# Kernel tuning notes

Hardware: AMD Instinct MI355X
Metric: run time of the kernel (lower is better)

The kernel has to match this reference:

```python
import jax, jax.numpy as jnp
import numpy as np

BLOCK = 192
SCALE = 2048 ** (-0.5)


def setup_inputs() -> dict:
    key = jax.random.key(0)
    k1, k2, k3, k4 = jax.random.split(key, 4)
    B, N, C = 8, 1920, 512
    x = jax.random.normal(k1, (B, N, C), dtype=jnp.float32)
    g = jax.random.normal(k2, (B, N, C), dtype=jnp.float32)
    # nn.Linear(dim, dim, bias=False) weights, stored as [out, in] like torch
    Wq = jax.random.normal(k3, (C, C), dtype=jnp.float32) * (1.0 / np.sqrt(C))
    Wg = jax.random.normal(k4, (C, C), dtype=jnp.float32) * (1.0 / np.sqrt(C))
    return {"x": x, "g": g, "Wq": Wq, "Wg": Wg}


def reference(x, g, Wq, Wg):
    B, N, C = g.shape
    # q = x + mean over tokens of g
    q = x + jnp.mean(g, axis=1, keepdims=True)
    rel_q = jnp.einsum('bnc,dc->bnd', q, Wq)  # Linear: y = x @ W^T
    # ---- block-local cosine attention over chunks of 192 tokens ----
    gb = g.reshape(B * N // BLOCK, BLOCK, C)
    norm = jnp.linalg.norm(gb, axis=-1, keepdims=True)
    rel = gb / jnp.maximum(norm, 1e-12)  # F.normalize(dim=-1)
    scores = jnp.einsum('bic,bjc->bij', rel, rel) * SCALE  # [nb,192,192]
    attn = jax.nn.softmax(scores, axis=-1)
    g2 = jnp.einsum('bij,bjc->bic', attn, gb).reshape(B, N, C)
    # ---- global cross attention ----
    rel_g = jnp.einsum('bnc,dc->bnd', g2, Wg)
    scores2 = jnp.einsum('bmc,bnc->bmn', rel_q, rel_g) * SCALE  # [B,M,N]
    attn2 = jax.nn.softmax(scores2, axis=-1)
    out = jnp.einsum('bmn,bnc->bmc', attn2, g2)
    return out
```

## Files before the change

kernel.cpp:

```cpp
#include <hip/hip_runtime.h>
#include <math.h>

constexpr int Bsz  = 8;
constexpr int Ntok = 1920;
constexpr int Cdim = 512;
constexpr int BLK  = 192;
constexpr int Mrows = Bsz * Ntok;
constexpr int NBLK  = Mrows / BLK;
constexpr float SCALE = 0.02209708691207961f;

typedef _Float16 half8 __attribute__((ext_vector_type(8)));
typedef float    f32x4 __attribute__((ext_vector_type(4)));

#define GLOAD_LDS16(gp, lp) __builtin_amdgcn_global_load_lds( \
    (const __attribute__((address_space(1))) void*)(gp),      \
    (__attribute__((address_space(3))) void*)(lp), 16, 0, 0)

__device__ inline unsigned short f2h(float f) {
    _Float16 h = (_Float16)f;
    return __builtin_bit_cast(unsigned short, h);
}
__device__ inline float h2f(unsigned short u) {
    return (float)__builtin_bit_cast(_Float16, u);
}

template<int BK> __device__ inline int smask(int r) {
    return (BK == 32) ? ((r & 3) ^ ((r >> 2) & 3)) : (r & 7);
}

template<int N> __device__ __forceinline__ void vm_wait() {
    if constexpr (N == 0)      asm volatile("s_waitcnt vmcnt(0)" ::: "memory");
    else if constexpr (N == 2) asm volatile("s_waitcnt vmcnt(2)" ::: "memory");
    else if constexpr (N == 4) asm volatile("s_waitcnt vmcnt(4)" ::: "memory");
    else if constexpr (N == 6) asm volatile("s_waitcnt vmcnt(6)" ::: "memory");
    else                       asm volatile("s_waitcnt vmcnt(8)" ::: "memory");
}

__global__ void mean_partial(const float* __restrict__ g, float* __restrict__ part) {
    int b = blockIdx.x, t = blockIdx.y, c = threadIdx.x;
    const float* p = g + ((size_t)b * Ntok + (size_t)t * 48) * Cdim + c;
    float s = 0.f;
    #pragma unroll 4
    for (int n = 0; n < 48; ++n) s += p[(size_t)n * Cdim];
    part[((size_t)b * 40 + t) * Cdim + c] = s;
}

__global__ void mean_final(const float* __restrict__ part, float* __restrict__ meang) {
    int b = blockIdx.x, c = threadIdx.x;
    float s = 0.f;
    for (int t = 0; t < 40; ++t) s += part[((size_t)b * 40 + t) * Cdim + c];
    meang[b * Cdim + c] = s * (1.0f / (float)Ntok);
}

__global__ void invnorm_k(const float* __restrict__ g, float* __restrict__ invn) {
    int wid = threadIdx.x >> 6, lane = threadIdx.x & 63;
    int row = blockIdx.x * 4 + wid;
    const float* p = g + (size_t)row * Cdim;
    float ss = 0.f;
    #pragma unroll
    for (int i = lane; i < Cdim; i += 64) { float v = p[i]; ss += v * v; }
    #pragma unroll
    for (int o = 1; o < 64; o <<= 1) ss += __shfl_xor(ss, o);
    if (lane == 0) {
        float n = sqrtf(ss);
        invn[row] = 1.0f / fmaxf(n, 1e-12f);
    }
}

__global__ void cvt_k(const float* __restrict__ src, const float* __restrict__ bias,
                      unsigned short* __restrict__ dst, int n4) {
    int i = blockIdx.x * 256 + threadIdx.x;
    if (i >= n4) return;
    float4 v = ((const float4*)src)[i];
    if (bias) {
        int b  = i / (Ntok * Cdim / 4);
        int c4 = (i & (Cdim / 4 - 1)) << 2;
        float4 bv = *(const float4*)&bias[b * Cdim + c4];
        v.x += bv.x; v.y += bv.y; v.z += bv.z; v.w += bv.w;
    }
    ushort4 h;
    h.x = f2h(v.x); h.y = f2h(v.y); h.z = f2h(v.z); h.w = f2h(v.w);
    ((ushort4*)dst)[i] = h;
}

__global__ __launch_bounds__(256) void transpose1(
    const unsigned short* __restrict__ in, unsigned short* __restrict__ out,
    int R, int C, long inB, long outB)
{
    int z = blockIdx.z;
    in  += (size_t)z * inB;
    out += (size_t)z * outB;
    __shared__ unsigned short th[64][68];
    int r0 = blockIdx.y * 64, c0 = blockIdx.x * 64;
    int tr = threadIdx.x >> 4, tc = (threadIdx.x & 15) * 4;
    for (int rr = tr; rr < 64; rr += 16) {
        ushort4 h = *(const ushort4*)&in[(size_t)(r0 + rr) * C + c0 + tc];
        th[tc + 0][rr] = h.x; th[tc + 1][rr] = h.y; th[tc + 2][rr] = h.z; th[tc + 3][rr] = h.w;
    }
    __syncthreads();
    for (int cc = tr; cc < 64; cc += 16) {
        ushort4 h = *(const ushort4*)&th[cc][tc];
        *(ushort4*)&out[(size_t)(c0 + cc) * R + r0 + tc] = h;
    }
}

template<int FM, int FN, int BK>
__global__ __launch_bounds__(256) void mfma_gemm(
    const unsigned short* __restrict__ A, const unsigned short* __restrict__ B,
    float* __restrict__ Of32, unsigned short* __restrict__ Oh,
    int N, int K, int ld,
    long aB, long bB, long oB,
    float alpha, const float* __restrict__ rs, const float* __restrict__ cs, int sB)
{
    constexpr int BM = FM * 32, BN = FN * 32;
    constexpr int RPC = 512 / BK;
    constexpr int LPR = BK / 8;
    constexpr int NCH = (BM + BN) / RPC;
    constexpr int CPW = NCH / 4;
    int z = blockIdx.z;

    int gx = gridDim.x;
    int nwg = gx * gridDim.y;
    int orig = blockIdx.y * gx + blockIdx.x;
    int q = nwg >> 3, r = nwg & 7;
    int xcd = orig & 7, idx = orig >> 3;
    int wgid = (xcd < r ? xcd * (q + 1) : r * (q + 1) + (xcd - r) * q) + idx;
    int m0 = (wgid / gx) * BM, n0 = (wgid % gx) * BN;

    __shared__ __align__(16) unsigned short As[2][BM * BK];
    __shared__ __align__(16) unsigned short Bs[2][BN * BK];

    int tid  = threadIdx.x;
    int lane = tid & 63, wid = tid >> 6;
    int wm = (wid >> 1) * (FM * 16), wn = (wid & 1) * (FN * 16);

    int srow = lane / LPR;
    int sgc  = (lane % LPR) ^ smask<BK>(srow);

    const unsigned short* csrc[CPW];
    unsigned short* cdst0[CPW];
    unsigned short* cdst1[CPW];
    #pragma unroll
    for (int i = 0; i < CPW; ++i) {
        int c = wid * CPW + i;
        if (c < BM / RPC) {
            csrc[i]  = A + (size_t)z * aB + (size_t)(m0 + c * RPC + srow) * ld + sgc * 8;
            cdst0[i] = &As[0][c * 512];
            cdst1[i] = &As[1][c * 512];
        } else {
            int cb = c - BM / RPC;
            csrc[i]  = B + (size_t)z * bB + (size_t)(n0 + cb * RPC + srow) * ld + sgc * 8;
            cdst0[i] = &Bs[0][cb * 512];
            cdst1[i] = &Bs[1][cb * 512];
        }
    }

    f32x4 acc[FM][FN] = {};
    int fr = lane & 15, kq = lane >> 4;

    const int nt = K / BK;
    #pragma unroll
    for (int i = 0; i < CPW; ++i) GLOAD_LDS16(csrc[i], cdst0[i]);
    #pragma unroll
    for (int i = 0; i < CPW; ++i) GLOAD_LDS16(csrc[i] + BK, cdst1[i]);

    for (int t = 0; t < nt; ++t) {
        int cur = t & 1;
        if (t + 1 < nt) vm_wait<CPW>(); else vm_wait<0>();
        __builtin_amdgcn_sched_barrier(0);
        __builtin_amdgcn_s_barrier();
        __builtin_amdgcn_sched_barrier(0);

        const unsigned short* Ab = As[cur];
        const unsigned short* Bb = Bs[cur];
        #pragma unroll
        for (int ks = 0; ks < BK / 32; ++ks) {
            int slot = ks * 4 + kq;
            half8 a[FM], b[FN];
            #pragma unroll
            for (int f = 0; f < FM; ++f) {
                int rr = wm + f * 16 + fr;
                a[f] = *(const half8*)&Ab[rr * BK + ((slot ^ smask<BK>(rr)) << 3)];
            }
            #pragma unroll
            for (int f = 0; f < FN; ++f) {
                int rr = wn + f * 16 + fr;
                b[f] = *(const half8*)&Bb[rr * BK + ((slot ^ smask<BK>(rr)) << 3)];
            }
            #pragma unroll
            for (int i = 0; i < FM; ++i)
                #pragma unroll
                for (int j = 0; j < FN; ++j)
                    acc[i][j] = __builtin_amdgcn_mfma_f32_16x16x32_f16(a[i], b[j], acc[i][j], 0, 0, 0);
        }

        __builtin_amdgcn_sched_barrier(0);
        __builtin_amdgcn_s_barrier();
        if (t + 2 < nt) {
            const int k2 = (t + 2) * BK;
            #pragma unroll
            for (int i = 0; i < CPW; ++i)
                GLOAD_LDS16(csrc[i] + k2, cur ? cdst1[i] : cdst0[i]);
        }
    }

    float* O          = Of32 ? Of32 + (size_t)z * oB : nullptr;
    unsigned short* H = Oh   ? Oh   + (size_t)z * oB : nullptr;
    int fq = lane >> 4;
    #pragma unroll
    for (int i = 0; i < FM; ++i) {
        #pragma unroll
        for (int r4 = 0; r4 < 4; ++r4) {
            int gm = m0 + wm + i * 16 + fq * 4 + r4;
            float rf = alpha * (rs ? rs[(size_t)z * sB + gm] : 1.0f);
            #pragma unroll
            for (int j = 0; j < FN; ++j) {
                int gn = n0 + wn + j * 16 + fr;
                float v = acc[i][j][r4] * rf * (cs ? cs[(size_t)z * sB + gn] : 1.0f);
                size_t off = (size_t)gm * N + gn;
                if (O) O[off] = v;
                else   H[off] = f2h(v);
            }
        }
    }
}

__global__ __launch_bounds__(512, 2) void gemm256(
    const unsigned short* __restrict__ A, const unsigned short* __restrict__ B,
    unsigned short* __restrict__ Oh,
    int M, int N, int K, int ld,
    long aB, long bB, long oB, float alpha)
{
    int z = blockIdx.z;
    int gx = gridDim.x;
    int nwg = gx * gridDim.y;
    int orig = blockIdx.y * gx + blockIdx.x;
    int q = nwg >> 3, r = nwg & 7;
    int xcd = orig & 7, idx = orig >> 3;
    int wgid = (xcd < r ? xcd * (q + 1) : r * (q + 1) + (xcd - r) * q) + idx;
    int m0 = (wgid / gx) * 256, n0 = (wgid % gx) * 256;

    __shared__ __align__(16) unsigned short As[2][256 * 64];
    __shared__ __align__(16) unsigned short Bs[2][256 * 64];

    int tid = threadIdx.x, lane = tid & 63, wid = tid >> 6;
    int wr = wid >> 2, wc = wid & 3;
    const unsigned short* Az = A + (size_t)z * aB;
    const unsigned short* Bz = B + (size_t)z * bB;

    int srow8 = lane >> 3;
    int sslot = (lane & 7) ^ srow8;

    auto stageT = [&](int t) {
        int cur = t & 1;
        const int koff = t * 64;
        #pragma unroll
        for (int i = 0; i < 4; ++i) {
            int c = wid * 4 + i;
            int rrow = c * 8 + srow8;
            int gr = min(m0 + rrow, M - 1);
            GLOAD_LDS16(Az + (size_t)gr * ld + koff + sslot * 8, &As[cur][c * 512]);
        }
        #pragma unroll
        for (int i = 0; i < 4; ++i) {
            int c = wid * 4 + i;
            int rrow = c * 8 + srow8;
            int gc = min(n0 + rrow, N - 1);
            GLOAD_LDS16(Bz + (size_t)gc * ld + koff + sslot * 8, &Bs[cur][c * 512]);
        }
    };

    f32x4 acc[8][4] = {};
    int fr = lane & 15, kq = lane >> 4;

    const int nt = K / 64;
    stageT(0);
    stageT(1);

    for (int t = 0; t < nt; ++t) {
        int cur = t & 1;
        if (t + 1 < nt) vm_wait<8>(); else vm_wait<0>();
        __builtin_amdgcn_sched_barrier(0);
        __builtin_amdgcn_s_barrier();
        __builtin_amdgcn_sched_barrier(0);

        const unsigned short* Ab = As[cur];
        const unsigned short* Bb = Bs[cur];
        __builtin_amdgcn_s_setprio(1);
        half8 b[4][2];
        #pragma unroll
        for (int nf = 0; nf < 4; ++nf) {
            int rr = wc * 64 + nf * 16 + fr;
            #pragma unroll
            for (int ks = 0; ks < 2; ++ks) {
                int slot = (ks * 4 + kq) ^ (rr & 7);
                b[nf][ks] = *(const half8*)&Bb[rr * 64 + slot * 8];
            }
        }
        #pragma unroll
        for (int mf = 0; mf < 8; ++mf) {
            int rr = wr * 128 + mf * 16 + fr;
            half8 a[2];
            #pragma unroll
            for (int ks = 0; ks < 2; ++ks) {
                int slot = (ks * 4 + kq) ^ (rr & 7);
                a[ks] = *(const half8*)&Ab[rr * 64 + slot * 8];
            }
            #pragma unroll
            for (int nf = 0; nf < 4; ++nf)
                #pragma unroll
                for (int ks = 0; ks < 2; ++ks)
                    acc[mf][nf] = __builtin_amdgcn_mfma_f32_16x16x32_f16(
                        a[ks], b[nf][ks], acc[mf][nf], 0, 0, 0);
        }
        __builtin_amdgcn_s_setprio(0);

        __builtin_amdgcn_sched_barrier(0);
        __builtin_amdgcn_s_barrier();
        __builtin_amdgcn_sched_barrier(0);
        if (t + 2 < nt) stageT(t + 2);
    }

    unsigned short* H = Oh + (size_t)z * oB;
    int fq = lane >> 4;
    #pragma unroll
    for (int mi = 0; mi < 8; ++mi) {
        #pragma unroll
        for (int r4 = 0; r4 < 4; ++r4) {
            int gm = m0 + wr * 128 + mi * 16 + fq * 4 + r4;
            if (gm >= M) continue;
            #pragma unroll
            for (int ni = 0; ni < 4; ++ni) {
                int gn = n0 + wc * 64 + ni * 16 + fr;
                if (gn >= N) continue;
                H[(size_t)gm * N + gn] = f2h(acc[mi][ni][r4] * alpha);
            }
        }
    }
}

__global__ __launch_bounds__(256) void softmax_h(unsigned short* __restrict__ P, int cols) {
    __shared__ float buf[1920];
    __shared__ float red[4];
    size_t row = blockIdx.x;
    unsigned short* p = P + row * (size_t)cols;
    int tid = threadIdx.x;
    int nq = cols >> 2;

    float lmax = -1e30f;
    for (int q = tid; q < nq; q += 256) {
        ushort4 h = ((const ushort4*)p)[q];
        float v0 = h2f(h.x), v1 = h2f(h.y), v2 = h2f(h.z), v3 = h2f(h.w);
        buf[q * 4 + 0] = v0; buf[q * 4 + 1] = v1;
        buf[q * 4 + 2] = v2; buf[q * 4 + 3] = v3;
        lmax = fmaxf(lmax, fmaxf(fmaxf(v0, v1), fmaxf(v2, v3)));
    }
    #pragma unroll
    for (int o = 1; o < 64; o <<= 1) lmax = fmaxf(lmax, __shfl_xor(lmax, o));
    if ((tid & 63) == 0) red[tid >> 6] = lmax;
    __syncthreads();
    float bmax = fmaxf(fmaxf(red[0], red[1]), fmaxf(red[2], red[3]));

    float lsum = 0.f;
    for (int c = tid; c < cols; c += 256) {
        float e = expf(buf[c] - bmax);
        buf[c] = e;
        lsum += e;
    }
    #pragma unroll
    for (int o = 1; o < 64; o <<= 1) lsum += __shfl_xor(lsum, o);
    __syncthreads();
    if ((tid & 63) == 0) red[tid >> 6] = lsum;
    __syncthreads();
    float inv = 1.0f / (red[0] + red[1] + red[2] + red[3]);

    for (int q = tid; q < nq; q += 256) {
        ushort4 h;
        h.x = f2h(buf[q * 4 + 0] * inv);
        h.y = f2h(buf[q * 4 + 1] * inv);
        h.z = f2h(buf[q * 4 + 2] * inv);
        h.w = f2h(buf[q * 4 + 3] * inv);
        ((ushort4*)p)[q] = h;
    }
}

extern "C" void kernel_launch(void* const* d_in, const int* in_sizes, int n_in,
                              void* d_out, int out_size, void* d_ws, size_t ws_size,
                              hipStream_t stream) {
    (void)in_sizes; (void)n_in; (void)out_size; (void)ws_size;
    const float* x  = (const float*)d_in[0];
    const float* g  = (const float*)d_in[1];
    const float* Wq = (const float*)d_in[2];
    const float* Wg = (const float*)d_in[3];
    float* out = (float*)d_out;

    const size_t GE = (size_t)Mrows * Cdim;
    char* ws = (char*)d_ws;
    size_t off = 0;
    auto alloc = [&](size_t bytes) { char* p = ws + off; off += (bytes + 255) & ~(size_t)255; return p; };

    float* meang = (float*)alloc(Bsz * Cdim * 4);
    float* part  = (float*)alloc(Bsz * 40 * Cdim * 4);
    float* invn  = (float*)alloc(Mrows * 4);
    unsigned short* gh   = (unsigned short*)alloc(GE * 2);
    unsigned short* gTh  = (unsigned short*)alloc(GE * 2);
    unsigned short* qh   = (unsigned short*)alloc(GE * 2);
    unsigned short* wqh  = (unsigned short*)alloc((size_t)Cdim * Cdim * 2);
    unsigned short* wgh  = (unsigned short*)alloc((size_t)Cdim * Cdim * 2);
    unsigned short* rqh  = (unsigned short*)alloc(GE * 2);
    unsigned short* rgh  = (unsigned short*)alloc(GE * 2);
    unsigned short* g2h  = (unsigned short*)alloc(GE * 2);
    unsigned short* sbh  = (unsigned short*)alloc((size_t)NBLK * BLK * BLK * 2);
    unsigned short* s2h  = (unsigned short*)alloc((size_t)Bsz * Ntok * Ntok * 2);
    unsigned short* g2Th = qh;

    mean_partial<<<dim3(Bsz, 40), 512, 0, stream>>>(g, part);
    mean_final<<<Bsz, 512, 0, stream>>>(part, meang);
    invnorm_k<<<Mrows / 4, 256, 0, stream>>>(g, invn);

    cvt_k<<<(int)(GE / 4 + 255) / 256, 256, 0, stream>>>(g, nullptr, gh, (int)(GE / 4));
    cvt_k<<<(int)(GE / 4 + 255) / 256, 256, 0, stream>>>(x, meang, qh, (int)(GE / 4));
    cvt_k<<<(Cdim * Cdim / 4) / 256, 256, 0, stream>>>(Wq, nullptr, wqh, Cdim * Cdim / 4);
    cvt_k<<<(Cdim * Cdim / 4) / 256, 256, 0, stream>>>(Wg, nullptr, wgh, Cdim * Cdim / 4);

    transpose1<<<dim3(Cdim / 64, BLK / 64, NBLK), 256, 0, stream>>>(
        gh, gTh, BLK, Cdim, (long)BLK * Cdim, (long)Cdim * BLK);

    mfma_gemm<2, 4, 64><<<dim3(Cdim / 128, Mrows / 64), 256, 0, stream>>>(
        qh, wqh, nullptr, rqh, Cdim, Cdim, Cdim, 0, 0, 0, 1.0f, nullptr, nullptr, 0);

    mfma_gemm<2, 2, 32><<<dim3(3, 3, NBLK), 256, 0, stream>>>(
        gh, gh, nullptr, sbh, BLK, Cdim, Cdim,
        (long)BLK * Cdim, (long)BLK * Cdim, (long)BLK * BLK,
        SCALE, invn, invn, BLK);

    softmax_h<<<NBLK * BLK, 256, 0, stream>>>(sbh, BLK);

    mfma_gemm<2, 4, 64><<<dim3(Cdim / 128, BLK / 64, NBLK), 256, 0, stream>>>(
        sbh, gTh, nullptr, g2h, Cdim, BLK, BLK,
        (long)BLK * BLK, (long)Cdim * BLK, (long)BLK * Cdim,
        1.0f, nullptr, nullptr, 0);

    transpose1<<<dim3(Cdim / 64, Ntok / 64, Bsz), 256, 0, stream>>>(
        g2h, g2Th, Ntok, Cdim, (long)Ntok * Cdim, (long)Cdim * Ntok);

    mfma_gemm<2, 4, 64><<<dim3(Cdim / 128, Mrows / 64), 256, 0, stream>>>(
        g2h, wgh, nullptr, rgh, Cdim, Cdim, Cdim, 0, 0, 0, 1.0f, nullptr, nullptr, 0);

    gemm256<<<dim3(8, 8, Bsz), 512, 0, stream>>>(
        rqh, rgh, s2h, Ntok, Ntok, Cdim, Cdim,
        (long)Ntok * Cdim, (long)Ntok * Cdim, (long)Ntok * Ntok, SCALE);

    softmax_h<<<Bsz * Ntok, 256, 0, stream>>>(s2h, Ntok);

    mfma_gemm<4, 4, 64><<<dim3(Cdim / 128, Ntok / 128, Bsz), 256, 0, stream>>>(
        s2h, g2Th, out, nullptr, Cdim, Ntok, Ntok,
        (long)Ntok * Ntok, (long)Cdim * Ntok, (long)Ntok * Cdim,
        1.0f, nullptr, nullptr, 0);
}
```

Before: 261.1 us.

## Switch GEMMs to BK=32 four-stage LDS ring with one barrier per step

Result: slower. 279.8 us (+7.1%).

```diff
diff --git a/kernel.cpp b/kernel.cpp
--- a/kernel.cpp
+++ b/kernel.cpp
@@ -24,13 +24,12 @@
     return (float)__builtin_bit_cast(_Float16, u);
 }
 
-template<int BK> __device__ inline int smask(int r) {
-    return (BK == 32) ? ((r & 3) ^ ((r >> 2) & 3)) : (r & 7);
-}
+__device__ inline int sfun32(int r) { return (r & 3) ^ ((r >> 2) & 3); }
 
 template<int N> __device__ __forceinline__ void vm_wait() {
     if constexpr (N == 0)      asm volatile("s_waitcnt vmcnt(0)" ::: "memory");
     else if constexpr (N == 2) asm volatile("s_waitcnt vmcnt(2)" ::: "memory");
+    else if constexpr (N == 3) asm volatile("s_waitcnt vmcnt(3)" ::: "memory");
     else if constexpr (N == 4) asm volatile("s_waitcnt vmcnt(4)" ::: "memory");
     else if constexpr (N == 6) asm volatile("s_waitcnt vmcnt(6)" ::: "memory");
     else                       asm volatile("s_waitcnt vmcnt(8)" ::: "memory");
@@ -104,7 +103,7 @@
     }
 }
 
-template<int FM, int FN, int BK>
+template<int FM, int FN>
 __global__ __launch_bounds__(256) void mfma_gemm(
     const unsigned short* __restrict__ A, const unsigned short* __restrict__ B,
     float* __restrict__ Of32, unsigned short* __restrict__ Oh,
@@ -113,10 +112,9 @@
     float alpha, const float* __restrict__ rs, const float* __restrict__ cs, int sB)
 {
     constexpr int BM = FM * 32, BN = FN * 32;
-    constexpr int RPC = 512 / BK;
-    constexpr int LPR = BK / 8;
-    constexpr int NCH = (BM + BN) / RPC;
+    constexpr int NCH = (BM + BN) / 16;
     constexpr int CPW = NCH / 4;
+    constexpr int ASZ = BM * 32, BSZ = BN * 32;
     int z = blockIdx.z;
 
     int gx = gridDim.x;
@@ -127,81 +125,82 @@
     int wgid = (xcd < r ? xcd * (q + 1) : r * (q + 1) + (xcd - r) * q) + idx;
     int m0 = (wgid / gx) * BM, n0 = (wgid % gx) * BN;
 
-    __shared__ __align__(16) unsigned short As[2][BM * BK];
-    __shared__ __align__(16) unsigned short Bs[2][BN * BK];
+    __shared__ __align__(16) unsigned short As[4][ASZ];
+    __shared__ __align__(16) unsigned short Bs[4][BSZ];
 
     int tid  = threadIdx.x;
     int lane = tid & 63, wid = tid >> 6;
     int wm = (wid >> 1) * (FM * 16), wn = (wid & 1) * (FN * 16);
 
-    int srow = lane / LPR;
-    int sgc  = (lane % LPR) ^ smask<BK>(srow);
+    int srow = lane >> 2;
+    int sgc  = (lane & 3) ^ sfun32(srow);
 
     const unsigned short* csrc[CPW];
-    unsigned short* cdst0[CPW];
-    unsigned short* cdst1[CPW];
+    unsigned short* cdst[CPW];
+    int cstep[CPW];
     #pragma unroll
     for (int i = 0; i < CPW; ++i) {
         int c = wid * CPW + i;
-        if (c < BM / RPC) {
-            csrc[i]  = A + (size_t)z * aB + (size_t)(m0 + c * RPC + srow) * ld + sgc * 8;
-            cdst0[i] = &As[0][c * 512];
-            cdst1[i] = &As[1][c * 512];
+        if (c < BM / 16) {
+            csrc[i]  = A + (size_t)z * aB + (size_t)(m0 + c * 16 + srow) * ld + sgc * 8;
+            cdst[i]  = &As[0][c * 512];
+            cstep[i] = ASZ;
         } else {
-            int cb = c - BM / RPC;
-            csrc[i]  = B + (size_t)z * bB + (size_t)(n0 + cb * RPC + srow) * ld + sgc * 8;
-            cdst0[i] = &Bs[0][cb * 512];
-            cdst1[i] = &Bs[1][cb * 512];
+            int cb = c - BM / 16;
+            csrc[i]  = B + (size_t)z * bB + (size_t)(n0 + cb * 16 + srow) * ld + sgc * 8;
+            cdst[i]  = &Bs[0][cb * 512];
+            cstep[i] = BSZ;
         }
     }
 
     f32x4 acc[FM][FN] = {};
     int fr = lane & 15, kq = lane >> 4;
 
-    const int nt = K / BK;
-    #pragma unroll
-    for (int i = 0; i < CPW; ++i) GLOAD_LDS16(csrc[i], cdst0[i]);
-    #pragma unroll
-    for (int i = 0; i < CPW; ++i) GLOAD_LDS16(csrc[i] + BK, cdst1[i]);
+    const int nt = K / 32;
+    #pragma unroll
+    for (int s = 0; s < 3; ++s)
+        #pragma unroll
+        for (int i = 0; i < CPW; ++i)
+            GLOAD_LDS16(csrc[i] + s * 32, cdst[i] + s * cstep[i]);
 
     for (int t = 0; t < nt; ++t) {
-        int cur = t & 1;
-        if (t + 1 < nt) vm_wait<CPW>(); else vm_wait<0>();
+        int rem = nt - 1 - t;
+        if (rem >= 2)      vm_wait<2 * CPW>();
+        else if (rem == 1) vm_wait<CPW>();
+        else               vm_wait<0>();
         __builtin_amdgcn_sched_barrier(0);
         __builtin_amdgcn_s_barrier();
         __builtin_amdgcn_sched_barrier(0);
 
-        const unsigned short* Ab = As[cur];
-        const unsigned short* Bb = Bs[cur];
-        #pragma unroll
-        for (int ks = 0; ks < BK / 32; ++ks) {
-            int slot = ks * 4 + kq;
-            half8 a[FM], b[FN];
-            #pragma unroll
-            for (int f = 0; f < FM; ++f) {
-                int rr = wm + f * 16 + fr;
-                a[f] = *(const half8*)&Ab[rr * BK + ((slot ^ smask<BK>(rr)) << 3)];
-            }
-            #pragma unroll
-            for (int f = 0; f < FN; ++f) {
-                int rr = wn + f * 16 + fr;
-                b[f] = *(const half8*)&Bb[rr * BK + ((slot ^ smask<BK>(rr)) << 3)];
-            }
-            #pragma unroll
-            for (int i = 0; i < FM; ++i)
-                #pragma unroll
-                for (int j = 0; j < FN; ++j)
-                    acc[i][j] = __builtin_amdgcn_mfma_f32_16x16x32_f16(a[i], b[j], acc[i][j], 0, 0, 0);
-        }
-
-        __builtin_amdgcn_sched_barrier(0);
-        __builtin_amdgcn_s_barrier();
-        if (t + 2 < nt) {
-            const int k2 = (t + 2) * BK;
+        if (t + 3 < nt) {
+            int b3 = (t + 3) & 3;
+            const int k3 = (t + 3) * 32;
             #pragma unroll
             for (int i = 0; i < CPW; ++i)
-                GLOAD_LDS16(csrc[i] + k2, cur ? cdst1[i] : cdst0[i]);
-        }
+                GLOAD_LDS16(csrc[i] + k3, cdst[i] + b3 * cstep[i]);
+        }
+
+        int cur = t & 3;
+        const unsigned short* Ab = &As[cur][0];
+        const unsigned short* Bb = &Bs[cur][0];
+        __builtin_amdgcn_s_setprio(1);
+        half8 a[FM], b[FN];
+        #pragma unroll
+        for (int f = 0; f < FN; ++f) {
+            int rr = wn + f * 16 + fr;
+            b[f] = *(const half8*)&Bb[rr * 32 + ((kq ^ sfun32(rr)) << 3)];
+        }
+        #pragma unroll
+        for (int f = 0; f < FM; ++f) {
+            int rr = wm + f * 16 + fr;
+            a[f] = *(const half8*)&Ab[rr * 32 + ((kq ^ sfun32(rr)) << 3)];
+        }
+        #pragma unroll
+        for (int i = 0; i < FM; ++i)
+            #pragma unroll
+            for (int j = 0; j < FN; ++j)
+                acc[i][j] = __builtin_amdgcn_mfma_f32_16x16x32_f16(a[i], b[j], acc[i][j], 0, 0, 0);
+        __builtin_amdgcn_s_setprio(0);
     }
 
     float* O          = Of32 ? Of32 + (size_t)z * oB : nullptr;
@@ -240,85 +239,71 @@
     int wgid = (xcd < r ? xcd * (q + 1) : r * (q + 1) + (xcd - r) * q) + idx;
     int m0 = (wgid / gx) * 256, n0 = (wgid % gx) * 256;
 
-    __shared__ __align__(16) unsigned short As[2][256 * 64];
-    __shared__ __align__(16) unsigned short Bs[2][256 * 64];
+    __shared__ __align__(16) unsigned short As[4][256 * 32];
+    __shared__ __align__(16) unsigned short Bs[4][256 * 32];
 
     int tid = threadIdx.x, lane = tid & 63, wid = tid >> 6;
     int wr = wid >> 2, wc = wid & 3;
     const unsigned short* Az = A + (size_t)z * aB;
     const unsigned short* Bz = B + (size_t)z * bB;
 
-    int srow8 = lane >> 3;
-    int sslot = (lane & 7) ^ srow8;
+    int srow = lane >> 2;
+    int sgc  = (lane & 3) ^ sfun32(srow);
 
     auto stageT = [&](int t) {
-        int cur = t & 1;
-        const int koff = t * 64;
+        int buf = t & 3;
+        const int koff = t * 32;
         #pragma unroll
         for (int i = 0; i < 4; ++i) {
             int c = wid * 4 + i;
-            int rrow = c * 8 + srow8;
-            int gr = min(m0 + rrow, M - 1);
-            GLOAD_LDS16(Az + (size_t)gr * ld + koff + sslot * 8, &As[cur][c * 512]);
-        }
-        #pragma unroll
-        for (int i = 0; i < 4; ++i) {
-            int c = wid * 4 + i;
-            int rrow = c * 8 + srow8;
-            int gc = min(n0 + rrow, N - 1);
-            GLOAD_LDS16(Bz + (size_t)gc * ld + koff + sslot * 8, &Bs[cur][c * 512]);
+            if (c < 16) {
+                int gr = min(m0 + c * 16 + srow, M - 1);
+                GLOAD_LDS16(Az + (size_t)gr * ld + koff + sgc * 8, &As[buf][c * 512]);
+            } else {
+                int cb = c - 16;
+                int gc = min(n0 + cb * 16 + srow, N - 1);
+                GLOAD_LDS16(Bz + (size_t)gc * ld + koff + sgc * 8, &Bs[buf][cb * 512]);
+            }
         }
     };
 
     f32x4 acc[8][4] = {};
     int fr = lane & 15, kq = lane >> 4;
 
-    const int nt = K / 64;
-    stageT(0);
-    stageT(1);
+    const int nt = K / 32;
+    stageT(0); stageT(1); stageT(2);
 
     for (int t = 0; t < nt; ++t) {
-        int cur = t & 1;
-        if (t + 1 < nt) vm_wait<8>(); else vm_wait<0>();
+        int rem = nt - 1 - t;
+        if (rem >= 2)      vm_wait<8>();
+        else if (rem == 1) vm_wait<4>();
+        else               vm_wait<0>();
         __builtin_amdgcn_sched_barrier(0);
         __builtin_amdgcn_s_barrier();
         __builtin_amdgcn_sched_barrier(0);
 
-        const unsigned short* Ab = As[cur];
-        const unsigned short* Bb = Bs[cur];
+        if (t + 3 < nt) stageT(t + 3);
+
+        int cur = t & 3;
+        const unsigned short* Ab = &As[cur][0];
+        const unsigned short* Bb = &Bs[cur][0];
         __builtin_amdgcn_s_setprio(1);
-        half8 b[4][2];
+        half8 b[4];
         #pragma unroll
         for (int nf = 0; nf < 4; ++nf) {
             int rr = wc * 64 + nf * 16 + fr;
-            #pragma unroll
-            for (int ks = 0; ks < 2; ++ks) {
-                int slot = (ks * 4 + kq) ^ (rr & 7);
-                b[nf][ks] = *(const half8*)&Bb[rr * 64 + slot * 8];
-            }
+            b[nf] = *(const half8*)&Bb[rr * 32 + ((kq ^ sfun32(rr)) << 3)];
         }
         #pragma unroll
         for (int mf = 0; mf < 8; ++mf) {
             int rr = wr * 128 + mf * 16 + fr;
-            half8 a[2];
-            #pragma unroll
-            for (int ks = 0; ks < 2; ++ks) {
-                int slot = (ks * 4 + kq) ^ (rr & 7);
-                a[ks] = *(const half8*)&Ab[rr * 64 + slot * 8];
-            }
+            half8 a = *(const half8*)&Ab[rr * 32 + ((kq ^ sfun32(rr)) << 3)];
             #pragma unroll
             for (int nf = 0; nf < 4; ++nf)
-                #pragma unroll
-                for (int ks = 0; ks < 2; ++ks)
-                    acc[mf][nf] = __builtin_amdgcn_mfma_f32_16x16x32_f16(
-                        a[ks], b[nf][ks], acc[mf][nf], 0, 0, 0);
+                acc[mf][nf] = __builtin_amdgcn_mfma_f32_16x16x32_f16(
+                    a, b[nf], acc[mf][nf], 0, 0, 0);
         }
         __builtin_amdgcn_s_setprio(0);
-
-        __builtin_amdgcn_sched_barrier(0);
-        __builtin_amdgcn_s_barrier();
-        __builtin_amdgcn_sched_barrier(0);
-        if (t + 2 < nt) stageT(t + 2);
     }
 
     unsigned short* H = Oh + (size_t)z * oB;
@@ -426,17 +411,17 @@
     transpose1<<<dim3(Cdim / 64, BLK / 64, NBLK), 256, 0, stream>>>(
         gh, gTh, BLK, Cdim, (long)BLK * Cdim, (long)Cdim * BLK);
 
-    mfma_gemm<2, 4, 64><<<dim3(Cdim / 128, Mrows / 64), 256, 0, stream>>>(
+    mfma_gemm<2, 4><<<dim3(Cdim / 128, Mrows / 64), 256, 0, stream>>>(
         qh, wqh, nullptr, rqh, Cdim, Cdim, Cdim, 0, 0, 0, 1.0f, nullptr, nullptr, 0);
 
-    mfma_gemm<2, 2, 32><<<dim3(3, 3, NBLK), 256, 0, stream>>>(
+    mfma_gemm<2, 2><<<dim3(3, 3, NBLK), 256, 0, stream>>>(
         gh, gh, nullptr, sbh, BLK, Cdim, Cdim,
         (long)BLK * Cdim, (long)BLK * Cdim, (long)BLK * BLK,
         SCALE, invn, invn, BLK);
 
     softmax_h<<<NBLK * BLK, 256, 0, stream>>>(sbh, BLK);
 
-    mfma_gemm<2, 4, 64><<<dim3(Cdim / 128, BLK / 64, NBLK), 256, 0, stream>>>(
+    mfma_gemm<2, 4><<<dim3(Cdim / 128, BLK / 64, NBLK), 256, 0, stream>>>(
         sbh, gTh, nullptr, g2h, Cdim, BLK, BLK,
         (long)BLK * BLK, (long)Cdim * BLK, (long)BLK * Cdim,
         1.0f, nullptr, nullptr, 0);
@@ -444,7 +429,7 @@
     transpose1<<<dim3(Cdim / 64, Ntok / 64, Bsz), 256, 0, stream>>>(
         g2h, g2Th, Ntok, Cdim, (long)Ntok * Cdim, (long)Cdim * Ntok);
 
-    mfma_gemm<2, 4, 64><<<dim3(Cdim / 128, Mrows / 64), 256, 0, stream>>>(
+    mfma_gemm<2, 4><<<dim3(Cdim / 128, Mrows / 64), 256, 0, stream>>>(
         g2h, wgh, nullptr, rgh, Cdim, Cdim, Cdim, 0, 0, 0, 1.0f, nullptr, nullptr, 0);
 
     gemm256<<<dim3(8, 8, Bsz), 512, 0, stream>>>(
@@ -453,7 +438,7 @@
 
     softmax_h<<<Bsz * Ntok, 256, 0, stream>>>(s2h, Ntok);
 
-    mfma_gemm<4, 4, 64><<<dim3(Cdim / 128, Ntok / 128, Bsz), 256, 0, stream>>>(
+    mfma_gemm<4, 4><<<dim3(Cdim / 128, Ntok / 128, Bsz), 256, 0, stream>>>(
         s2h, g2Th, out, nullptr, Cdim, Ntok, Ntok,
         (long)Ntok * Ntok, (long)Cdim * Ntok, (long)Ntok * Cdim,
         1.0f, nullptr, nullptr, 0);
```

## Fuse global softmax exp and partial row sums into score GEMM epilogue

Applied to the files above, without the earlier changes.

Result: faster. 239.5 us (-8.3%).

```diff
diff --git a/kernel.cpp b/kernel.cpp
--- a/kernel.cpp
+++ b/kernel.cpp
@@ -227,7 +227,7 @@
 
 __global__ __launch_bounds__(512, 2) void gemm256(
     const unsigned short* __restrict__ A, const unsigned short* __restrict__ B,
-    unsigned short* __restrict__ Oh,
+    unsigned short* __restrict__ Oh, float* __restrict__ psum,
     int M, int N, int K, int ld,
     long aB, long bB, long oB, float alpha)
 {
@@ -238,7 +238,8 @@
     int q = nwg >> 3, r = nwg & 7;
     int xcd = orig & 7, idx = orig >> 3;
     int wgid = (xcd < r ? xcd * (q + 1) : r * (q + 1) + (xcd - r) * q) + idx;
-    int m0 = (wgid / gx) * 256, n0 = (wgid % gx) * 256;
+    int bx = wgid % gx;
+    int m0 = (wgid / gx) * 256, n0 = bx * 256;
 
     __shared__ __align__(16) unsigned short As[2][256 * 64];
     __shared__ __align__(16) unsigned short Bs[2][256 * 64];
@@ -328,15 +329,36 @@
         #pragma unroll
         for (int r4 = 0; r4 < 4; ++r4) {
             int gm = m0 + wr * 128 + mi * 16 + fq * 4 + r4;
-            if (gm >= M) continue;
+            bool vrow = gm < M;
+            float rsum = 0.f;
             #pragma unroll
             for (int ni = 0; ni < 4; ++ni) {
                 int gn = n0 + wc * 64 + ni * 16 + fr;
-                if (gn >= N) continue;
-                H[(size_t)gm * N + gn] = f2h(acc[mi][ni][r4] * alpha);
-            }
-        }
-    }
+                float e = __expf(acc[mi][ni][r4] * alpha);
+                unsigned short eh = f2h(e);
+                if (vrow && gn < N) {
+                    H[(size_t)gm * N + gn] = eh;
+                    rsum += h2f(eh);
+                }
+            }
+            rsum += __shfl_xor(rsum, 1);
+            rsum += __shfl_xor(rsum, 2);
+            rsum += __shfl_xor(rsum, 4);
+            rsum += __shfl_xor(rsum, 8);
+            if (vrow && fr == 0)
+                psum[((size_t)z * M + gm) * 32 + bx * 4 + wc] = rsum;
+        }
+    }
+}
+
+__global__ void rowsum_inv(const float* __restrict__ ps, float* __restrict__ inv, int rows) {
+    int i = blockIdx.x * 256 + threadIdx.x;
+    if (i >= rows) return;
+    const float* p = ps + (size_t)i * 32;
+    float s = 0.f;
+    #pragma unroll
+    for (int j = 0; j < 32; ++j) s += p[j];
+    inv[i] = 1.0f / s;
 }
 
 __global__ __launch_bounds__(256) void softmax_h(unsigned short* __restrict__ P, int cols) {
@@ -412,6 +434,8 @@
     unsigned short* g2h  = (unsigned short*)alloc(GE * 2);
     unsigned short* sbh  = (unsigned short*)alloc((size_t)NBLK * BLK * BLK * 2);
     unsigned short* s2h  = (unsigned short*)alloc((size_t)Bsz * Ntok * Ntok * 2);
+    float* psum  = (float*)alloc((size_t)Mrows * 32 * 4);
+    float* rsinv = (float*)alloc((size_t)Mrows * 4);
     unsigned short* g2Th = qh;
 
     mean_partial<<<dim3(Bsz, 40), 512, 0, stream>>>(g, part);
@@ -448,13 +472,13 @@
         g2h, wgh, nullptr, rgh, Cdim, Cdim, Cdim, 0, 0, 0, 1.0f, nullptr, nullptr, 0);
 
     gemm256<<<dim3(8, 8, Bsz), 512, 0, stream>>>(
-        rqh, rgh, s2h, Ntok, Ntok, Cdim, Cdim,
+        rqh, rgh, s2h, psum, Ntok, Ntok, Cdim, Cdim,
         (long)Ntok * Cdim, (long)Ntok * Cdim, (long)Ntok * Ntok, SCALE);
 
-    softmax_h<<<Bsz * Ntok, 256, 0, stream>>>(s2h, Ntok);
+    rowsum_inv<<<(Mrows + 255) / 256, 256, 0, stream>>>(psum, rsinv, Mrows);
 
     mfma_gemm<4, 4, 64><<<dim3(Cdim / 128, Ntok / 128, Bsz), 256, 0, stream>>>(
         s2h, g2Th, out, nullptr, Cdim, Ntok, Ntok,
         (long)Ntok * Ntok, (long)Cdim * Ntok, (long)Ntok * Cdim,
-        1.0f, nullptr, nullptr, 0);
-}
+        1.0f, rsinv, nullptr, Ntok);
+}
```
